# Performance work log

Measured on AMD Instinct MI355X. Metric: run time of the kernel, lower is better.

The kernel has to match this reference:

```python
import jax, jax.numpy as jnp
import numpy as np

NUM_CLASS = 19
N_PIX = 262144  # 2 * 256 * 512 flattened pixels per domain
D_FEAT = 256


def setup_inputs() -> dict:
    key = jax.random.key(0)
    ks = jax.random.split(key, 6)
    return {
        "source_feat": jax.random.normal(ks[0], (N_PIX, D_FEAT), jnp.float32),
        "target_feat": jax.random.normal(ks[1], (N_PIX, D_FEAT), jnp.float32),
        "target_conf": jax.random.uniform(ks[2], (N_PIX,), jnp.float32),
        "source_argmax": jax.random.randint(ks[3], (N_PIX,), 0, NUM_CLASS, jnp.int32),
        "target_argmax": jax.random.randint(ks[4], (N_PIX,), 0, NUM_CLASS, jnp.int32),
        "source_mask": jax.random.randint(ks[5], (N_PIX,), 0, 2, jnp.int32).astype(bool),
    }


def _masked_entropy(z, seen):
    # entropy term sum(p * log p) over seen classes only (unseen logits = -inf)
    z = jnp.where(seen[None, :], z, -jnp.inf)
    logp = jax.nn.log_softmax(z, axis=1)
    p = jnp.exp(logp)
    return jnp.sum(jnp.where(seen[None, :], p * logp, 0.0), axis=1)


def reference(source_feat, target_feat, target_conf, source_argmax, target_argmax, source_mask):
    C = NUM_CLASS
    seg = jax.ops.segment_sum
    w_s = source_mask.astype(source_feat.dtype)          # confident source pixels weight 1
    w_t = 1.0 - target_conf                              # target weight = 1 - confidence

    # ---- compute_centroids_mixed: per-class weighted sum over both domains ----
    sum_c = (seg(source_feat * w_s[:, None], source_argmax, C)
             + seg(target_feat * w_t[:, None], target_argmax, C))       # [C, D]
    denom = seg(w_s, source_argmax, C) + seg(w_t, target_argmax, C)     # [C]
    seen = denom > 0
    centroids = jnp.where(seen[:, None], sum_c / jnp.maximum(denom, 1e-12)[:, None], jnp.inf)
    cent_safe = jnp.where(seen[:, None], centroids, 0.0)                # for matmul

    # ---- similarity_dsb('both', temperature=1.0) ----
    # original gathers masked source rows; equivalent: weight unmasked rows 0 and
    # divide by (#masked source + #target) instead of taking a plain mean.
    z_s = source_feat @ cent_safe.T                                     # [Ns, C]
    z_t = target_feat @ cent_safe.T                                     # [Nt, C]
    ent_s = _masked_entropy(z_s, seen)
    ent_t = _masked_entropy(z_t, seen)
    w_t_sim = 1.0 - jax.lax.stop_gradient(target_conf)  # detached in similarity_dsb
    total = jnp.sum(w_s * ent_s) + jnp.sum(w_t_sim * ent_t)
    n = jnp.sum(w_s) + jnp.asarray(target_feat.shape[0], source_feat.dtype)
    loss = -total / n

    return jnp.concatenate([centroids.reshape(-1), loss[None]])
```

## Files before the change

### kernel.cpp

```cpp
#include <hip/hip_runtime.h>

#define NPIX 262144
#define NCLS 19
#define DF 256
#define REPL 16

#define OFF_SUM  0
#define OFF_DEN  77824
#define OFF_WSUM 78128
#define OFF_TOT  78144
#define OFF_SEEN 78160
#define OFF_CENT 78176
#define MEMSET_BYTES (OFF_CENT * 4)

__global__ __launch_bounds__(256) void k_phase1(
    const float* __restrict__ sfeat, const float* __restrict__ tfeat,
    const float* __restrict__ conf, const int* __restrict__ sarg,
    const int* __restrict__ targ, const int* __restrict__ smask,
    float* __restrict__ ws)
{
    __shared__ float buf0[NCLS * DF];
    __shared__ float buf1[NCLS * DF];
    __shared__ float lden[NCLS];
    const int t = threadIdx.x;
    if (t < NCLS) lden[t] = 0.f;
    __syncthreads();

    const int lane = t & 63;
    const int wv = t >> 6;
    const int iBase = blockIdx.x * 128 + wv * 32;

    const int il = iBase + (lane >> 1);
    int cl; float wtl;
    if (lane & 1) { cl = targ[il]; wtl = 1.f - conf[il]; }
    else          { cl = sarg[il]; wtl = smask[il] ? 1.f : 0.f; }
    atomicAdd(&lden[cl], wtl);
    float wloc = (lane & 1) ? 0.f : wtl;

    float acc[NCLS][4];
    #pragma unroll
    for (int c = 0; c < NCLS; ++c)
        acc[c][0] = acc[c][1] = acc[c][2] = acc[c][3] = 0.f;

    const float4* sf = (const float4*)(sfeat + (size_t)iBase * DF);
    const float4* tf = (const float4*)(tfeat + (size_t)iBase * DF);

    #pragma unroll 4
    for (int it = 0; it < 32; ++it) {
        const int   c0 = __shfl(cl,  2 * it);
        const float w0 = __shfl(wtl, 2 * it);
        const int   c1 = __shfl(cl,  2 * it + 1);
        const float w1 = __shfl(wtl, 2 * it + 1);
        const float4 f0 = sf[it * 64 + lane];
        const float4 f1 = tf[it * 64 + lane];
        #pragma unroll
        for (int c = 0; c < NCLS; ++c) {
            const float ws0 = (c0 == c) ? w0 : 0.f;
            const float ws1 = (c1 == c) ? w1 : 0.f;
            acc[c][0] += ws0 * f0.x + ws1 * f1.x;
            acc[c][1] += ws0 * f0.y + ws1 * f1.y;
            acc[c][2] += ws0 * f0.z + ws1 * f1.z;
            acc[c][3] += ws0 * f0.w + ws1 * f1.w;
        }
    }

    float4* b = (float4*)((wv & 1) ? buf1 : buf0);
    if (wv < 2) {
        #pragma unroll
        for (int c = 0; c < NCLS; ++c)
            b[c * 64 + lane] = make_float4(acc[c][0], acc[c][1], acc[c][2], acc[c][3]);
    }
    __syncthreads();
    if (wv >= 2) {
        #pragma unroll
        for (int c = 0; c < NCLS; ++c) {
            float4 v = b[c * 64 + lane];
            v.x += acc[c][0]; v.y += acc[c][1]; v.z += acc[c][2]; v.w += acc[c][3];
            b[c * 64 + lane] = v;
        }
    }

    wloc += __shfl_xor(wloc, 32); wloc += __shfl_xor(wloc, 16);
    wloc += __shfl_xor(wloc, 8);  wloc += __shfl_xor(wloc, 4);
    wloc += __shfl_xor(wloc, 2);  wloc += __shfl_xor(wloc, 1);
    const int rep = blockIdx.x & (REPL - 1);
    if (lane == 0) unsafeAtomicAdd(&ws[OFF_WSUM + rep], wloc);
    __syncthreads();

    float* gsum = ws + OFF_SUM + rep * (NCLS * DF);
    for (int j = t; j < NCLS * DF; j += 256) {
        const float v = buf0[j] + buf1[j];
        if (v != 0.f) unsafeAtomicAdd(&gsum[j], v);
    }
    if (t < NCLS) unsafeAtomicAdd(&ws[OFF_DEN + rep * NCLS + t], lden[t]);
}

__global__ __launch_bounds__(256) void k_centroids(float* __restrict__ ws,
                                                   float* __restrict__ out)
{
    const int c = blockIdx.x;
    const int d = threadIdx.x;
    float den = 0.f;
    for (int r = 0; r < REPL; ++r) den += ws[OFF_DEN + r * NCLS + c];
    const bool seen = den > 0.f;
    float s = 0.f;
    for (int r = 0; r < REPL; ++r) s += ws[OFF_SUM + r * (NCLS * DF) + c * DF + d];
    const float centv = seen ? s / fmaxf(den, 1e-12f) : __builtin_inff();
    out[c * DF + d] = centv;
    ws[OFF_CENT + c * DF + d] = seen ? centv : 0.f;
    if (d == 0 && seen) atomicOr((int*)ws + OFF_SEEN, 1 << c);
}

__global__ __launch_bounds__(256) void k_entropy(
    const float* __restrict__ sfeat, const float* __restrict__ tfeat,
    const float* __restrict__ conf, const int* __restrict__ smask,
    float* __restrict__ ws)
{
    __shared__ float cent[NCLS * DF];
    __shared__ int seenSh;
    __shared__ float wacc[4];
    const int t = threadIdx.x;
    for (int j = t; j < NCLS * DF; j += 256) cent[j] = ws[OFF_CENT + j];
    if (t == 0) seenSh = ((const int*)ws)[OFF_SEEN];
    __syncthreads();
    const int seenM = seenSh;

    const int lane = t & 63, wv = t >> 6;
    const int sub = lane & 3, grp = lane >> 2;
    const int iBase = blockIdx.x * 128 + wv * 32 + grp * 2;

    const float w0 = smask[iBase]     ? 1.f : 0.f;
    const float w1 = 1.f - conf[iBase];
    const float w2 = smask[iBase + 1] ? 1.f : 0.f;
    const float w3 = 1.f - conf[iBase + 1];

    const float4* r0 = (const float4*)(sfeat + (size_t)iBase * DF);
    const float4* r1 = (const float4*)(tfeat + (size_t)iBase * DF);
    const float4* r2 = (const float4*)(sfeat + (size_t)(iBase + 1) * DF);
    const float4* r3 = (const float4*)(tfeat + (size_t)(iBase + 1) * DF);
    const float4* cv = (const float4*)cent;

    float z0[NCLS], z1[NCLS], z2[NCLS], z3[NCLS];
    #pragma unroll
    for (int c = 0; c < NCLS; ++c) { z0[c]=0.f; z1[c]=0.f; z2[c]=0.f; z3[c]=0.f; }

    #pragma unroll 2
    for (int q = 0; q < 16; ++q) {
        const int o = sub + 4 * q;
        const float4 f0 = r0[o];
        const float4 f1 = r1[o];
        const float4 f2 = r2[o];
        const float4 f3 = r3[o];
        #pragma unroll
        for (int c = 0; c < NCLS; ++c) {
            const float4 cc = cv[c * 64 + o];
            z0[c] += f0.x*cc.x + f0.y*cc.y + f0.z*cc.z + f0.w*cc.w;
            z1[c] += f1.x*cc.x + f1.y*cc.y + f1.z*cc.z + f1.w*cc.w;
            z2[c] += f2.x*cc.x + f2.y*cc.y + f2.z*cc.z + f2.w*cc.w;
            z3[c] += f3.x*cc.x + f3.y*cc.y + f3.z*cc.z + f3.w*cc.w;
        }
    }

    const bool s1b = (sub & 1) != 0;
    const bool s2b = (sub & 2) != 0;
    float zm[NCLS];
    #pragma unroll
    for (int c = 0; c < NCLS; ++c) {
        float a  = s1b ? z1[c] : z0[c];
        float b  = s1b ? z0[c] : z1[c];
        a += __shfl_xor(b, 1);
        float a2 = s1b ? z3[c] : z2[c];
        float b2 = s1b ? z2[c] : z3[c];
        a2 += __shfl_xor(b2, 1);
        float k  = s2b ? a2 : a;
        float s  = s2b ? a  : a2;
        zm[c] = k + __shfl_xor(s, 2);
    }

    const float wme = s1b ? (s2b ? w3 : w1) : (s2b ? w2 : w0);
    float m = -3.4e38f;
    #pragma unroll
    for (int c = 0; c < NCLS; ++c)
        if ((seenM >> c) & 1) m = fmaxf(m, zm[c]);
    float ssum = 0.f, t1 = 0.f;
    #pragma unroll
    for (int c = 0; c < NCLS; ++c)
        if ((seenM >> c) & 1) {
            const float e = __expf(zm[c] - m);
            ssum += e; t1 += e * (zm[c] - m);
        }
    const float ent = t1 / ssum - __logf(ssum);
    float acc = (wme != 0.f) ? wme * ent : 0.f;

    acc += __shfl_xor(acc, 32); acc += __shfl_xor(acc, 16);
    acc += __shfl_xor(acc, 8);  acc += __shfl_xor(acc, 4);
    acc += __shfl_xor(acc, 2);  acc += __shfl_xor(acc, 1);
    if (lane == 0) wacc[wv] = acc;
    __syncthreads();
    if (t == 0)
        unsafeAtomicAdd(&ws[OFF_TOT + (blockIdx.x & (REPL - 1))],
                        wacc[0] + wacc[1] + wacc[2] + wacc[3]);
}

__global__ void k_loss(const float* __restrict__ ws, float* __restrict__ out)
{
    if (threadIdx.x == 0 && blockIdx.x == 0) {
        float tot = 0.f, wsum = 0.f;
        for (int r = 0; r < REPL; ++r) { tot += ws[OFF_TOT + r]; wsum += ws[OFF_WSUM + r]; }
        out[NCLS * DF] = -tot / (wsum + (float)NPIX);
    }
}

extern "C" void kernel_launch(void* const* d_in, const int* in_sizes, int n_in,
                              void* d_out, int out_size, void* d_ws, size_t ws_size,
                              hipStream_t stream)
{
    const float* sfeat = (const float*)d_in[0];
    const float* tfeat = (const float*)d_in[1];
    const float* conf  = (const float*)d_in[2];
    const int*   sarg  = (const int*)d_in[3];
    const int*   targ  = (const int*)d_in[4];
    const int*   smask = (const int*)d_in[5];
    float* out = (float*)d_out;
    float* ws  = (float*)d_ws;

    hipMemsetAsync(d_ws, 0, MEMSET_BYTES, stream);
    k_phase1   <<<2048, 256, 0, stream>>>(sfeat, tfeat, conf, sarg, targ, smask, ws);
    k_centroids<<<NCLS, 256, 0, stream>>>(ws, out);
    k_entropy  <<<2048, 256, 0, stream>>>(sfeat, tfeat, conf, smask, ws);
    k_loss     <<<1,    64,  0, stream>>>(ws, out);
}
```

Before: 726.3 us.

## Skip masked-out source rows, halve LDS buffers, use readlane for broadcasts

In phase 1, the source feature row is loaded and accumulated only when its mask weight is nonzero, which avoids reading about half of the source feature memory. Per-pixel class and weight broadcasts now use wave-uniform readlane instead of shuffles. The two LDS reduction buffers are merged into one, filled by a serialized four-wave accumulation, and a launch-bounds occupancy hint of 5 is added. The extra syncs and the divergent-free but data-dependent branch add overhead, and the occupancy hint may force register spills given the large accumulator array.

After: 872.5 us. +20.1%, slower.

```diff
diff --git a/kernel.cpp b/kernel.cpp
--- a/kernel.cpp
+++ b/kernel.cpp
@@ -13,14 +13,13 @@
 #define OFF_CENT 78176
 #define MEMSET_BYTES (OFF_CENT * 4)
 
-__global__ __launch_bounds__(256) void k_phase1(
+__global__ __launch_bounds__(256, 5) void k_phase1(
     const float* __restrict__ sfeat, const float* __restrict__ tfeat,
     const float* __restrict__ conf, const int* __restrict__ sarg,
     const int* __restrict__ targ, const int* __restrict__ smask,
     float* __restrict__ ws)
 {
-    __shared__ float buf0[NCLS * DF];
-    __shared__ float buf1[NCLS * DF];
+    __shared__ float lsum[NCLS * DF];
     __shared__ float lden[NCLS];
     const int t = threadIdx.x;
     if (t < NCLS) lden[t] = 0.f;
@@ -36,6 +35,7 @@
     else          { cl = sarg[il]; wtl = smask[il] ? 1.f : 0.f; }
     atomicAdd(&lden[cl], wtl);
     float wloc = (lane & 1) ? 0.f : wtl;
+    const int wti = __float_as_int(wtl);
 
     float acc[NCLS][4];
     #pragma unroll
@@ -47,36 +47,64 @@
 
     #pragma unroll 4
     for (int it = 0; it < 32; ++it) {
-        const int   c0 = __shfl(cl,  2 * it);
-        const float w0 = __shfl(wtl, 2 * it);
-        const int   c1 = __shfl(cl,  2 * it + 1);
-        const float w1 = __shfl(wtl, 2 * it + 1);
-        const float4 f0 = sf[it * 64 + lane];
+        const int   c1 = __builtin_amdgcn_readlane(cl,  2 * it + 1);
+        const float w1 = __int_as_float(__builtin_amdgcn_readlane(wti, 2 * it + 1));
+        const int   c0 = __builtin_amdgcn_readlane(cl,  2 * it);
+        const float w0 = __int_as_float(__builtin_amdgcn_readlane(wti, 2 * it));
+
         const float4 f1 = tf[it * 64 + lane];
         #pragma unroll
         for (int c = 0; c < NCLS; ++c) {
-            const float ws0 = (c0 == c) ? w0 : 0.f;
-            const float ws1 = (c1 == c) ? w1 : 0.f;
-            acc[c][0] += ws0 * f0.x + ws1 * f1.x;
-            acc[c][1] += ws0 * f0.y + ws1 * f1.y;
-            acc[c][2] += ws0 * f0.z + ws1 * f1.z;
-            acc[c][3] += ws0 * f0.w + ws1 * f1.w;
-        }
-    }
-
-    float4* b = (float4*)((wv & 1) ? buf1 : buf0);
-    if (wv < 2) {
+            const float s1 = (c1 == c) ? w1 : 0.f;
+            acc[c][0] += s1 * f1.x;
+            acc[c][1] += s1 * f1.y;
+            acc[c][2] += s1 * f1.z;
+            acc[c][3] += s1 * f1.w;
+        }
+        if (w0 != 0.f) {
+            const float4 f0 = sf[it * 64 + lane];
+            #pragma unroll
+            for (int c = 0; c < NCLS; ++c) {
+                const float s0 = (c0 == c) ? w0 : 0.f;
+                acc[c][0] += s0 * f0.x;
+                acc[c][1] += s0 * f0.y;
+                acc[c][2] += s0 * f0.z;
+                acc[c][3] += s0 * f0.w;
+            }
+        }
+    }
+
+    float4* lb = (float4*)lsum;
+    if (wv == 0) {
         #pragma unroll
         for (int c = 0; c < NCLS; ++c)
-            b[c * 64 + lane] = make_float4(acc[c][0], acc[c][1], acc[c][2], acc[c][3]);
-    }
-    __syncthreads();
-    if (wv >= 2) {
-        #pragma unroll
-        for (int c = 0; c < NCLS; ++c) {
-            float4 v = b[c * 64 + lane];
+            lb[c * 64 + lane] = make_float4(acc[c][0], acc[c][1], acc[c][2], acc[c][3]);
+    }
+    __syncthreads();
+    if (wv == 1) {
+        #pragma unroll
+        for (int c = 0; c < NCLS; ++c) {
+            float4 v = lb[c * 64 + lane];
             v.x += acc[c][0]; v.y += acc[c][1]; v.z += acc[c][2]; v.w += acc[c][3];
-            b[c * 64 + lane] = v;
+            lb[c * 64 + lane] = v;
+        }
+    }
+    __syncthreads();
+    if (wv == 2) {
+        #pragma unroll
+        for (int c = 0; c < NCLS; ++c) {
+            float4 v = lb[c * 64 + lane];
+            v.x += acc[c][0]; v.y += acc[c][1]; v.z += acc[c][2]; v.w += acc[c][3];
+            lb[c * 64 + lane] = v;
+        }
+    }
+    __syncthreads();
+    if (wv == 3) {
+        #pragma unroll
+        for (int c = 0; c < NCLS; ++c) {
+            float4 v = lb[c * 64 + lane];
+            v.x += acc[c][0]; v.y += acc[c][1]; v.z += acc[c][2]; v.w += acc[c][3];
+            lb[c * 64 + lane] = v;
         }
     }
 
@@ -84,12 +112,13 @@
     wloc += __shfl_xor(wloc, 8);  wloc += __shfl_xor(wloc, 4);
     wloc += __shfl_xor(wloc, 2);  wloc += __shfl_xor(wloc, 1);
     const int rep = blockIdx.x & (REPL - 1);
+    if (lane == 0 && wv == 0) ;
     if (lane == 0) unsafeAtomicAdd(&ws[OFF_WSUM + rep], wloc);
     __syncthreads();
 
     float* gsum = ws + OFF_SUM + rep * (NCLS * DF);
     for (int j = t; j < NCLS * DF; j += 256) {
-        const float v = buf0[j] + buf1[j];
+        const float v = lsum[j];
         if (v != 0.f) unsafeAtomicAdd(&gsum[j], v);
     }
     if (t < NCLS) unsafeAtomicAdd(&ws[OFF_DEN + rep * NCLS + t], lden[t]);
```
